# Optimization experiments

Hardware: AMD Instinct MI355X
Metric: run time of the kernel (lower is better)

Reference implementation:

```python
import math
import jax, jax.numpy as jnp
import numpy as np

B, C, H, W = 4, 64, 128, 128
A = 64           # attention_size
OUT = 64         # output_size
KS = 3           # kernel_size
M = (KS - 1) // 2
SCALE = A ** (-0.5)


def _lin(x, Wt, b):
    return x @ Wt + b


def _pos_encoding(d_model, seq_len):
    # sinusoidal PE over the k^2 neighborhood positions; d_model even here
    pos = jnp.arange(seq_len, dtype=jnp.float32)[:, None]
    div = jnp.exp(jnp.arange(0, d_model, 2, dtype=jnp.float32) * (-math.log(10000.0) / d_model))
    s = jnp.sin(pos * div)   # (seq, d/2)
    c = jnp.cos(pos * div)
    return jnp.stack([s, c], axis=-1).reshape(seq_len, d_model)  # interleaved sin/cos


def _expand_shift(k_nchw):
    # k_nchw: (b, c, h, w) -> (b, c, h, w, KS*KS) neighbor gather (zero padded)
    h, w = k_nchw.shape[2], k_nchw.shape[3]
    p = jnp.pad(k_nchw, ((0, 0), (0, 0), (M, M), (M, M)))
    slices = [p[:, :, i:i + h, j:j + w] for i in range(KS) for j in range(KS)]
    return jnp.stack(slices, axis=-1)


def setup_inputs() -> dict:
    key = jax.random.key(0)
    ks = jax.random.split(key, 12)
    sd = lambda fan_in: 1.0 / math.sqrt(fan_in)
    return {
        "x": jax.random.normal(ks[0], (B, C, H, W), jnp.float32),
        "ln_g": jnp.ones((C,), jnp.float32),
        "ln_b": jnp.zeros((C,), jnp.float32),
        "Wq": jax.random.normal(ks[1], (C, 2 * A), jnp.float32) * sd(C),
        "bq": jnp.zeros((2 * A,), jnp.float32),
        "Wq2": jax.random.normal(ks[2], (2 * A, A), jnp.float32) * sd(2 * A),
        "bq2": jnp.zeros((A,), jnp.float32),
        "Wk": jax.random.normal(ks[3], (C, 2 * A), jnp.float32) * sd(C),
        "bk": jnp.zeros((2 * A,), jnp.float32),
        "Wk2": jax.random.normal(ks[4], (2 * A, A), jnp.float32) * sd(2 * A),
        "bk2": jnp.zeros((A,), jnp.float32),
        "Wv": jax.random.normal(ks[5], (C, 2 * A), jnp.float32) * sd(C),
        "bv": jnp.zeros((2 * A,), jnp.float32),
        "Wv2": jax.random.normal(ks[6], (2 * A, OUT), jnp.float32) * sd(2 * A),
        "bv2": jnp.zeros((OUT,), jnp.float32),
        "Wpos": jax.random.normal(ks[7], (C, A), jnp.float32) * sd(C),
        "bpos": jnp.zeros((A,), jnp.float32),
        "Wposk": jax.random.normal(ks[8], (A, A), jnp.float32) * sd(A),
        "bposk": jnp.zeros((A,), jnp.float32),
    }


def reference(x, ln_g, ln_b, Wq, bq, Wq2, bq2, Wk, bk, Wk2, bk2,
              Wv, bv, Wv2, bv2, Wpos, bpos, Wposk, bposk):
    # positional embedding over the 9 neighborhood slots
    pe = _pos_encoding(C, KS * KS)                       # (9, C)
    pos_emb = jax.nn.relu(_lin(pe, Wpos, bpos))          # (9, A)

    xn = jnp.transpose(x, (0, 2, 3, 1))                  # (b, h, w, c)
    mu = jnp.mean(xn, axis=-1, keepdims=True)
    var = jnp.mean((xn - mu) ** 2, axis=-1, keepdims=True)
    xn = (xn - mu) * jax.lax.rsqrt(var + 1e-5) * ln_g + ln_b

    K = _lin(jax.nn.relu(_lin(xn, Wk, bk)), Wk2, bk2)    # (b, h, w, A)
    Ksh = _expand_shift(jnp.transpose(K, (0, 3, 1, 2)))  # (b, A, h, w, 9)
    pos_k = jnp.transpose(_lin(pos_emb, Wposk, bposk))   # (A, 9)
    Kfull = Ksh + pos_k[None, :, None, None, :]

    Q = _lin(jax.nn.relu(_lin(xn, Wq, bq)), Wq2, bq2)    # (b, h, w, A)
    V = _lin(jax.nn.relu(_lin(xn, Wv, bv)), Wv2, bv2)    # (b, h, w, OUT)
    Vsh = _expand_shift(jnp.transpose(V, (0, 3, 1, 2)))  # (b, OUT, h, w, 9)

    att = jnp.einsum('bhwa,bahwp->bphw', Q, Kfull) * SCALE
    att = jax.nn.softmax(att, axis=1)                    # softmax over 9 neighbors
    out = jnp.einsum('bchwn,bnhw->bchw', Vsh, att)       # (b, OUT, h, w)
    return out  # stride == 1 -> no subsampling
```

## Files before the change

kernel.cpp:

```cpp
#include <hip/hip_runtime.h>
#include <hip/hip_bf16.h>
#include <math.h>

typedef __attribute__((ext_vector_type(8))) short short8;
typedef __attribute__((ext_vector_type(4))) float float4v;
typedef unsigned short ushort_t;
typedef unsigned int uint_t;

#define HWPIX 16384
#define NPIX  65536

__device__ inline float b2f(ushort_t u) {
    uint_t x = ((uint_t)u) << 16;
    return __builtin_bit_cast(float, x);
}
__device__ inline ushort_t f2b(float f) {
    uint_t x = __builtin_bit_cast(uint_t, f);
    uint_t r = (x + 0x7fffu + ((x >> 16) & 1u)) >> 16;
    return (ushort_t)r;
}
__device__ inline uint_t pack2(float a, float b) {
    return (uint_t)f2b(a) | ((uint_t)f2b(b) << 16);
}
__device__ inline bool probe_bf16(const void* lng) {
    return *(const uint_t*)lng == 0x3F803F80u;
}
__device__ inline float ldf(const void* p, int i, bool bf) {
    return bf ? b2f(((const ushort_t*)p)[i]) : ((const float*)p)[i];
}
__device__ inline void unpack8(uint4 u, float* f) {
    f[0] = b2f((ushort_t)(u.x & 0xffff)); f[1] = b2f((ushort_t)(u.x >> 16));
    f[2] = b2f((ushort_t)(u.y & 0xffff)); f[3] = b2f((ushort_t)(u.y >> 16));
    f[4] = b2f((ushort_t)(u.z & 0xffff)); f[5] = b2f((ushort_t)(u.z >> 16));
    f[6] = b2f((ushort_t)(u.w & 0xffff)); f[7] = b2f((ushort_t)(u.w >> 16));
}

__global__ __launch_bounds__(256) void prep_kernel(
        const void* __restrict__ Wq, const void* __restrict__ Wq2,
        const void* __restrict__ Wk, const void* __restrict__ Wk2,
        const void* __restrict__ Wv, const void* __restrict__ Wv2,
        const void* __restrict__ Wpos, const void* __restrict__ bpos,
        const void* __restrict__ Wposk, const void* __restrict__ bposk,
        const void* __restrict__ lng,
        ushort_t* __restrict__ W1A, ushort_t* __restrict__ W2A, float* __restrict__ pk) {
    bool bf = probe_bf16(lng);
    if (blockIdx.x < 96) {
        int idx = blockIdx.x * 256 + threadIdx.x;
        int chain = idx >> 13;
        int o = idx & 8191;
        const void* W1 = chain == 0 ? Wq : (chain == 1 ? Wk : Wv);
        const void* W2 = chain == 0 ? Wq2 : (chain == 1 ? Wk2 : Wv2);
        {
            int j = o & 7, L = (o >> 3) & 63, kc = (o >> 9) & 1, mt = (o >> 10) & 7;
            int k = kc * 32 + ((L >> 4) << 3) + j;
            int m = mt * 16 + (L & 15);
            W1A[chain * 8192 + o] = f2b(ldf(W1, k * 128 + m, bf));
        }
        {
            int j = o & 7, L = (o >> 3) & 63, kc = (o >> 9) & 3, mt2 = (o >> 11) & 3;
            int k = kc * 32 + ((L >> 4) << 3) + j;
            int m = mt2 * 16 + (L & 15);
            W2A[chain * 8192 + o] = f2b(ldf(W2, k * 64 + m, bf));
        }
    } else {
        __shared__ float pe[9][64];
        __shared__ float pemb[9][64];
        int t = threadIdx.x;
        for (int it = t; it < 576; it += 256) {
            int p = it >> 6, a = it & 63;
            int i = a >> 1;
            float div = expf(-(float)(2 * i) * 0.14391156831212787f);
            float ang = (float)p * div;
            pe[p][a] = (a & 1) ? cosf(ang) : sinf(ang);
        }
        __syncthreads();
        for (int it = t; it < 576; it += 256) {
            int p = it >> 6, a = it & 63;
            float s = ldf(bpos, a, bf);
            for (int c = 0; c < 64; ++c) s += pe[p][c] * ldf(Wpos, c * 64 + a, bf);
            pemb[p][a] = fmaxf(s, 0.f);
        }
        __syncthreads();
        for (int it = t; it < 576; it += 256) {
            int p = it >> 6, a = it & 63;
            float s = ldf(bposk, a, bf);
            for (int j = 0; j < 64; ++j) s += pemb[p][j] * ldf(Wposk, j * 64 + a, bf);
            pk[a * 9 + p] = s;
        }
    }
}

__global__ __launch_bounds__(256) void lnqkv_kernel(
        const void* __restrict__ x, const void* __restrict__ g, const void* __restrict__ bb,
        const ushort_t* __restrict__ W1A, const ushort_t* __restrict__ W2A,
        const void* __restrict__ b1q, const void* __restrict__ b1k, const void* __restrict__ b1v,
        const void* __restrict__ b2q, const void* __restrict__ b2k, const void* __restrict__ b2v,
        const void* __restrict__ lng,
        ushort_t* __restrict__ Qo, ushort_t* __restrict__ Ko, ushort_t* __restrict__ Vo) {
    bool bf = probe_bf16(lng);
    int tid = threadIdx.x;
    int wave = tid >> 6, lane = tid & 63;
    int q = lane >> 4, r = lane & 15;
    int base = blockIdx.x * 256 + wave * 64;
    int b = base >> 14;
    int spBase = base & 16383;

    short8 bfr[4][2];
#pragma unroll
    for (int t = 0; t < 4; ++t) {
        int sp = spBase + t * 16 + r;
        float xl[8], xh[8];
        if (bf) {
            const ushort_t* xb = (const ushort_t*)x + (size_t)b * 64 * HWPIX + sp;
#pragma unroll
            for (int j = 0; j < 8; ++j) {
                xl[j] = b2f(xb[(size_t)(q * 8 + j) * HWPIX]);
                xh[j] = b2f(xb[(size_t)(32 + q * 8 + j) * HWPIX]);
            }
        } else {
            const float* xb = (const float*)x + (size_t)b * 64 * HWPIX + sp;
#pragma unroll
            for (int j = 0; j < 8; ++j) {
                xl[j] = xb[(size_t)(q * 8 + j) * HWPIX];
                xh[j] = xb[(size_t)(32 + q * 8 + j) * HWPIX];
            }
        }
        float s1 = 0.f, s2 = 0.f;
#pragma unroll
        for (int j = 0; j < 8; ++j) {
            s1 += xl[j] + xh[j];
            s2 += xl[j] * xl[j] + xh[j] * xh[j];
        }
        s1 += __shfl_xor(s1, 16); s2 += __shfl_xor(s2, 16);
        s1 += __shfl_xor(s1, 32); s2 += __shfl_xor(s2, 32);
        float mu = s1 * (1.f / 64.f);
        float var = s2 * (1.f / 64.f) - mu * mu;
        float rstd = rsqrtf(var + 1e-5f);
#pragma unroll
        for (int j = 0; j < 8; ++j) {
            int c = q * 8 + j;
            bfr[t][0][j] = (short)f2b((xl[j] - mu) * rstd * ldf(g, c, bf) + ldf(bb, c, bf));
            bfr[t][1][j] = (short)f2b((xh[j] - mu) * rstd * ldf(g, c + 32, bf) + ldf(bb, c + 32, bf));
        }
    }

    __shared__ __align__(16) ushort_t hid[4][4][16][128];

#pragma unroll 1
    for (int chain = 0; chain < 3; ++chain) {
        const ushort_t* W1 = W1A + chain * 8192;
        const ushort_t* W2 = W2A + chain * 8192;
        const void* b1 = chain == 0 ? b1q : (chain == 1 ? b1k : b1v);
        const void* b2 = chain == 0 ? b2q : (chain == 1 ? b2k : b2v);
        ushort_t* out = chain == 0 ? Qo : (chain == 1 ? Ko : Vo);

        {
            short8 w1[8][2];
#pragma unroll
            for (int mt = 0; mt < 8; ++mt)
#pragma unroll
                for (int kc = 0; kc < 2; ++kc)
                    w1[mt][kc] = *reinterpret_cast<const short8*>(W1 + ((mt * 2 + kc) * 64 + lane) * 8);
#pragma unroll
            for (int mt = 0; mt < 8; ++mt) {
                float bias0 = ldf(b1, mt * 16 + q * 4 + 0, bf);
                float bias1 = ldf(b1, mt * 16 + q * 4 + 1, bf);
                float bias2 = ldf(b1, mt * 16 + q * 4 + 2, bf);
                float bias3 = ldf(b1, mt * 16 + q * 4 + 3, bf);
#pragma unroll
                for (int t = 0; t < 4; ++t) {
                    float4v acc = {0.f, 0.f, 0.f, 0.f};
                    acc = __builtin_amdgcn_mfma_f32_16x16x32_bf16(w1[mt][0], bfr[t][0], acc, 0, 0, 0);
                    acc = __builtin_amdgcn_mfma_f32_16x16x32_bf16(w1[mt][1], bfr[t][1], acc, 0, 0, 0);
                    float v0 = fmaxf(acc[0] + bias0, 0.f);
                    float v1 = fmaxf(acc[1] + bias1, 0.f);
                    float v2 = fmaxf(acc[2] + bias2, 0.f);
                    float v3 = fmaxf(acc[3] + bias3, 0.f);
                    int chunk = (2 * mt + (q >> 1)) ^ r;
                    ushort_t* dst = &hid[wave][t][r][0] + chunk * 8 + (q & 1) * 4;
                    uint2 d; d.x = pack2(v0, v1); d.y = pack2(v2, v3);
                    *reinterpret_cast<uint2*>(dst) = d;
                }
            }
        }
        {
            short8 w2[4][4];
#pragma unroll
            for (int mt2 = 0; mt2 < 4; ++mt2)
#pragma unroll
                for (int kc = 0; kc < 4; ++kc)
                    w2[mt2][kc] = *reinterpret_cast<const short8*>(W2 + ((mt2 * 4 + kc) * 64 + lane) * 8);
            short8 h2[4][4];
#pragma unroll
            for (int t = 0; t < 4; ++t)
#pragma unroll
                for (int kc = 0; kc < 4; ++kc) {
                    int chunk = (4 * kc + q) ^ r;
                    h2[t][kc] = *reinterpret_cast<const short8*>(&hid[wave][t][r][0] + chunk * 8);
                }
#pragma unroll
            for (int mt2 = 0; mt2 < 4; ++mt2) {
                float bias0 = ldf(b2, mt2 * 16 + q * 4 + 0, bf);
                float bias1 = ldf(b2, mt2 * 16 + q * 4 + 1, bf);
                float bias2 = ldf(b2, mt2 * 16 + q * 4 + 2, bf);
                float bias3 = ldf(b2, mt2 * 16 + q * 4 + 3, bf);
#pragma unroll
                for (int t = 0; t < 4; ++t) {
                    float4v acc = {0.f, 0.f, 0.f, 0.f};
#pragma unroll
                    for (int kc = 0; kc < 4; ++kc)
                        acc = __builtin_amdgcn_mfma_f32_16x16x32_bf16(w2[mt2][kc], h2[t][kc], acc, 0, 0, 0);
                    uint2 d;
                    d.x = pack2(acc[0] + bias0, acc[1] + bias1);
                    d.y = pack2(acc[2] + bias2, acc[3] + bias3);
                    int pixel = base + t * 16 + r;
                    *reinterpret_cast<uint2*>(out + (size_t)pixel * 64 + mt2 * 16 + q * 4) = d;
                }
            }
        }
    }
}

__global__ __launch_bounds__(256) void attn_kernel(
        const ushort_t* __restrict__ Q, const ushort_t* __restrict__ K,
        const ushort_t* __restrict__ V, const float* __restrict__ pk,
        const void* __restrict__ lng, void* __restrict__ out) {
    bool bf = probe_bf16(lng);
    int p = blockIdx.x * 256 + threadIdx.x;
    int b = p >> 14;
    int sp = p & 16383;
    int h = sp >> 7, w = sp & 127;

    float v64[64];
    const ushort_t* qp = Q + (size_t)p * 64;
#pragma unroll
    for (int c0 = 0; c0 < 64; c0 += 8) {
        uint4 u = *reinterpret_cast<const uint4*>(qp + c0);
        unpack8(u, &v64[c0]);
    }

    float s[9];
#pragma unroll
    for (int n = 0; n < 9; ++n) {
        int dy = n / 3 - 1, dx = n % 3 - 1;
        int hh = h + dy, ww = w + dx;
        float dot = 0.f;
#pragma unroll
        for (int c = 0; c < 64; ++c) dot += v64[c] * pk[c * 9 + n];
        if (hh >= 0 && hh < 128 && ww >= 0 && ww < 128) {
            const ushort_t* kp = K + ((size_t)(b << 14) + (size_t)(hh * 128 + ww)) * 64;
#pragma unroll
            for (int c0 = 0; c0 < 64; c0 += 8) {
                uint4 u = *reinterpret_cast<const uint4*>(kp + c0);
                float kv[8];
                unpack8(u, kv);
#pragma unroll
                for (int j = 0; j < 8; ++j) dot += v64[c0 + j] * kv[j];
            }
        }
        s[n] = dot * 0.125f;
    }
    float m = s[0];
#pragma unroll
    for (int n = 1; n < 9; ++n) m = fmaxf(m, s[n]);
    float sum = 0.f;
#pragma unroll
    for (int n = 0; n < 9; ++n) { s[n] = expf(s[n] - m); sum += s[n]; }
    float inv = 1.f / sum;

#pragma unroll
    for (int c = 0; c < 64; ++c) v64[c] = 0.f;
#pragma unroll
    for (int n = 0; n < 9; ++n) {
        int dy = n / 3 - 1, dx = n % 3 - 1;
        int hh = h + dy, ww = w + dx;
        if (hh < 0 || hh >= 128 || ww < 0 || ww >= 128) continue;
        float a = s[n] * inv;
        const ushort_t* vp = V + ((size_t)(b << 14) + (size_t)(hh * 128 + ww)) * 64;
#pragma unroll
        for (int c0 = 0; c0 < 64; c0 += 8) {
            uint4 u = *reinterpret_cast<const uint4*>(vp + c0);
            float vv[8];
            unpack8(u, vv);
#pragma unroll
            for (int j = 0; j < 8; ++j) v64[c0 + j] += a * vv[j];
        }
    }
    if (bf) {
        ushort_t* ob = (ushort_t*)out + ((size_t)b * 64) * HWPIX + sp;
#pragma unroll
        for (int c = 0; c < 64; ++c) ob[(size_t)c * HWPIX] = f2b(v64[c]);
    } else {
        float* ob = (float*)out + ((size_t)b * 64) * HWPIX + sp;
#pragma unroll
        for (int c = 0; c < 64; ++c) ob[(size_t)c * HWPIX] = v64[c];
    }
}

extern "C" void kernel_launch(void* const* d_in, const int* in_sizes, int n_in,
                              void* d_out, int out_size, void* d_ws, size_t ws_size,
                              hipStream_t stream) {
    (void)in_sizes; (void)n_in; (void)out_size; (void)ws_size;
    const void* x     = d_in[0];
    const void* ln_g  = d_in[1];
    const void* ln_b  = d_in[2];
    const void* Wq    = d_in[3];
    const void* bq    = d_in[4];
    const void* Wq2   = d_in[5];
    const void* bq2   = d_in[6];
    const void* Wk    = d_in[7];
    const void* bk    = d_in[8];
    const void* Wk2   = d_in[9];
    const void* bk2   = d_in[10];
    const void* Wv    = d_in[11];
    const void* bv    = d_in[12];
    const void* Wv2   = d_in[13];
    const void* bv2   = d_in[14];
    const void* Wpos  = d_in[15];
    const void* bpos  = d_in[16];
    const void* Wposk = d_in[17];
    const void* bposk = d_in[18];

    char* ws = (char*)d_ws;
    ushort_t* Qo  = (ushort_t*)(ws);
    ushort_t* Ko  = (ushort_t*)(ws + (size_t)8 * 1024 * 1024);
    ushort_t* Vo  = (ushort_t*)(ws + (size_t)16 * 1024 * 1024);
    ushort_t* W1A = (ushort_t*)(ws + (size_t)24 * 1024 * 1024);
    ushort_t* W2A = (ushort_t*)(ws + (size_t)24 * 1024 * 1024 + 65536);
    float*    pk  = (float*)(ws + (size_t)24 * 1024 * 1024 + 131072);

    prep_kernel<<<97, 256, 0, stream>>>(Wq, Wq2, Wk, Wk2, Wv, Wv2,
                                        Wpos, bpos, Wposk, bposk, ln_g, W1A, W2A, pk);
    lnqkv_kernel<<<256, 256, 0, stream>>>(x, ln_g, ln_b, W1A, W2A,
                                          bq, bk, bv, bq2, bk2, bv2, ln_g, Qo, Ko, Vo);
    attn_kernel<<<256, 256, 0, stream>>>(Qo, Ko, Vo, pk, ln_g, d_out);
}
```

Baseline: 177.9 us.

## Compute positional Q·posK scores via MFMA in QKV kernel, halve pixels per block

Moves the per-pixel dot product of Q with the 9 positional key vectors out of the attention kernel's scalar loop and into the QKV kernel. There it is computed with two bf16 MFMAs from the Q tile staged in shared memory and stored as a 16-float score per pixel. The QKV kernel also processes 32 pixels per wave instead of 64, doubling its grid to 512 blocks for more parallelism. The bf16 unpack helper is simplified to use bit shifts and masks. The trade-offs are an extra 4 MB buffer written and then read back, and the positional term now being rounded to bf16.

Result: no change. 176.0 us (-1.1%).

```diff
diff --git a/kernel.cpp b/kernel.cpp
--- a/kernel.cpp
+++ b/kernel.cpp
@@ -28,11 +28,13 @@
 __device__ inline float ldf(const void* p, int i, bool bf) {
     return bf ? b2f(((const ushort_t*)p)[i]) : ((const float*)p)[i];
 }
+__device__ inline float lo2f(uint_t u) { return __builtin_bit_cast(float, u << 16); }
+__device__ inline float hi2f(uint_t u) { return __builtin_bit_cast(float, u & 0xffff0000u); }
 __device__ inline void unpack8(uint4 u, float* f) {
-    f[0] = b2f((ushort_t)(u.x & 0xffff)); f[1] = b2f((ushort_t)(u.x >> 16));
-    f[2] = b2f((ushort_t)(u.y & 0xffff)); f[3] = b2f((ushort_t)(u.y >> 16));
-    f[4] = b2f((ushort_t)(u.z & 0xffff)); f[5] = b2f((ushort_t)(u.z >> 16));
-    f[6] = b2f((ushort_t)(u.w & 0xffff)); f[7] = b2f((ushort_t)(u.w >> 16));
+    f[0] = lo2f(u.x); f[1] = hi2f(u.x);
+    f[2] = lo2f(u.y); f[3] = hi2f(u.y);
+    f[4] = lo2f(u.z); f[5] = hi2f(u.z);
+    f[6] = lo2f(u.w); f[7] = hi2f(u.w);
 }
 
 __global__ __launch_bounds__(256) void prep_kernel(
@@ -42,7 +44,7 @@
         const void* __restrict__ Wpos, const void* __restrict__ bpos,
         const void* __restrict__ Wposk, const void* __restrict__ bposk,
         const void* __restrict__ lng,
-        ushort_t* __restrict__ W1A, ushort_t* __restrict__ W2A, float* __restrict__ pk) {
+        ushort_t* __restrict__ W1A, ushort_t* __restrict__ W2A, ushort_t* __restrict__ pkA) {
     bool bf = probe_bf16(lng);
     if (blockIdx.x < 96) {
         int idx = blockIdx.x * 256 + threadIdx.x;
@@ -65,6 +67,7 @@
     } else {
         __shared__ float pe[9][64];
         __shared__ float pemb[9][64];
+        __shared__ float pks[64][9];
         int t = threadIdx.x;
         for (int it = t; it < 576; it += 256) {
             int p = it >> 6, a = it & 63;
@@ -85,7 +88,17 @@
             int p = it >> 6, a = it & 63;
             float s = ldf(bposk, a, bf);
             for (int j = 0; j < 64; ++j) s += pemb[p][j] * ldf(Wposk, j * 64 + a, bf);
-            pk[a * 9 + p] = s;
+            pks[a][p] = s;
+        }
+        __syncthreads();
+        if (t < 128) {
+            int kc = t >> 6, L = t & 63;
+            int m = L & 15;
+#pragma unroll
+            for (int j = 0; j < 8; ++j) {
+                int k = kc * 32 + ((L >> 4) << 3) + j;
+                pkA[(kc * 64 + L) * 8 + j] = (m < 9) ? f2b(pks[k][m]) : (ushort_t)0;
+            }
         }
     }
 }
@@ -93,21 +106,26 @@
 __global__ __launch_bounds__(256) void lnqkv_kernel(
         const void* __restrict__ x, const void* __restrict__ g, const void* __restrict__ bb,
         const ushort_t* __restrict__ W1A, const ushort_t* __restrict__ W2A,
+        const ushort_t* __restrict__ pkAp,
         const void* __restrict__ b1q, const void* __restrict__ b1k, const void* __restrict__ b1v,
         const void* __restrict__ b2q, const void* __restrict__ b2k, const void* __restrict__ b2v,
         const void* __restrict__ lng,
-        ushort_t* __restrict__ Qo, ushort_t* __restrict__ Ko, ushort_t* __restrict__ Vo) {
+        ushort_t* __restrict__ Qo, ushort_t* __restrict__ Ko, ushort_t* __restrict__ Vo,
+        float* __restrict__ Spos) {
     bool bf = probe_bf16(lng);
     int tid = threadIdx.x;
     int wave = tid >> 6, lane = tid & 63;
     int q = lane >> 4, r = lane & 15;
-    int base = blockIdx.x * 256 + wave * 64;
+    int base = blockIdx.x * 128 + wave * 32;
     int b = base >> 14;
     int spBase = base & 16383;
 
-    short8 bfr[4][2];
-#pragma unroll
-    for (int t = 0; t < 4; ++t) {
+    short8 pkA0 = *reinterpret_cast<const short8*>(pkAp + (0 * 64 + lane) * 8);
+    short8 pkA1 = *reinterpret_cast<const short8*>(pkAp + (1 * 64 + lane) * 8);
+
+    short8 bfr[2][2];
+#pragma unroll
+    for (int t = 0; t < 2; ++t) {
         int sp = spBase + t * 16 + r;
         float xl[8], xh[8];
         if (bf) {
@@ -144,7 +162,7 @@
         }
     }
 
-    __shared__ __align__(16) ushort_t hid[4][4][16][128];
+    __shared__ __align__(16) ushort_t hid[4][2][16][128];
 
 #pragma unroll 1
     for (int chain = 0; chain < 3; ++chain) {
@@ -168,7 +186,7 @@
                 float bias2 = ldf(b1, mt * 16 + q * 4 + 2, bf);
                 float bias3 = ldf(b1, mt * 16 + q * 4 + 3, bf);
 #pragma unroll
-                for (int t = 0; t < 4; ++t) {
+                for (int t = 0; t < 2; ++t) {
                     float4v acc = {0.f, 0.f, 0.f, 0.f};
                     acc = __builtin_amdgcn_mfma_f32_16x16x32_bf16(w1[mt][0], bfr[t][0], acc, 0, 0, 0);
                     acc = __builtin_amdgcn_mfma_f32_16x16x32_bf16(w1[mt][1], bfr[t][1], acc, 0, 0, 0);
@@ -190,9 +208,9 @@
 #pragma unroll
                 for (int kc = 0; kc < 4; ++kc)
                     w2[mt2][kc] = *reinterpret_cast<const short8*>(W2 + ((mt2 * 4 + kc) * 64 + lane) * 8);
-            short8 h2[4][4];
-#pragma unroll
-            for (int t = 0; t < 4; ++t)
+            short8 h2[2][4];
+#pragma unroll
+            for (int t = 0; t < 2; ++t)
 #pragma unroll
                 for (int kc = 0; kc < 4; ++kc) {
                     int chunk = (4 * kc + q) ^ r;
@@ -205,7 +223,7 @@
                 float bias2 = ldf(b2, mt2 * 16 + q * 4 + 2, bf);
                 float bias3 = ldf(b2, mt2 * 16 + q * 4 + 3, bf);
 #pragma unroll
-                for (int t = 0; t < 4; ++t) {
+                for (int t = 0; t < 2; ++t) {
                     float4v acc = {0.f, 0.f, 0.f, 0.f};
 #pragma unroll
                     for (int kc = 0; kc < 4; ++kc)
@@ -215,7 +233,33 @@
                     d.y = pack2(acc[2] + bias2, acc[3] + bias3);
                     int pixel = base + t * 16 + r;
                     *reinterpret_cast<uint2*>(out + (size_t)pixel * 64 + mt2 * 16 + q * 4) = d;
-                }
+                    if (chain == 0) {
+                        int chunk = (2 * mt2 + (q >> 1)) ^ r;
+                        ushort_t* dst = &hid[wave][t][r][0] + chunk * 8 + (q & 1) * 4;
+                        *reinterpret_cast<uint2*>(dst) = d;
+                    }
+                }
+            }
+        }
+        if (chain == 0) {
+#pragma unroll
+            for (int t = 0; t < 2; ++t) {
+                short8 qB0, qB1;
+                {
+                    int chunk = (4 * 0 + q) ^ r;
+                    qB0 = *reinterpret_cast<const short8*>(&hid[wave][t][r][0] + chunk * 8);
+                }
+                {
+                    int chunk = (4 * 1 + q) ^ r;
+                    qB1 = *reinterpret_cast<const short8*>(&hid[wave][t][r][0] + chunk * 8);
+                }
+                float4v acc = {0.f, 0.f, 0.f, 0.f};
+                acc = __builtin_amdgcn_mfma_f32_16x16x32_bf16(pkA0, qB0, acc, 0, 0, 0);
+                acc = __builtin_amdgcn_mfma_f32_16x16x32_bf16(pkA1, qB1, acc, 0, 0, 0);
+                int pixel = base + t * 16 + r;
+                float4 o;
+                o.x = acc[0]; o.y = acc[1]; o.z = acc[2]; o.w = acc[3];
+                *reinterpret_cast<float4*>(Spos + (size_t)pixel * 16 + q * 4) = o;
             }
         }
     }
@@ -223,7 +267,7 @@
 
 __global__ __launch_bounds__(256) void attn_kernel(
         const ushort_t* __restrict__ Q, const ushort_t* __restrict__ K,
-        const ushort_t* __restrict__ V, const float* __restrict__ pk,
+        const ushort_t* __restrict__ V, const float* __restrict__ Spos,
         const void* __restrict__ lng, void* __restrict__ out) {
     bool bf = probe_bf16(lng);
     int p = blockIdx.x * 256 + threadIdx.x;
@@ -240,13 +284,18 @@
     }
 
     float s[9];
+    {
+        float4 s0 = *reinterpret_cast<const float4*>(Spos + (size_t)p * 16);
+        float4 s1 = *reinterpret_cast<const float4*>(Spos + (size_t)p * 16 + 4);
+        s[0] = s0.x; s[1] = s0.y; s[2] = s0.z; s[3] = s0.w;
+        s[4] = s1.x; s[5] = s1.y; s[6] = s1.z; s[7] = s1.w;
+        s[8] = Spos[(size_t)p * 16 + 8];
+    }
 #pragma unroll
     for (int n = 0; n < 9; ++n) {
         int dy = n / 3 - 1, dx = n % 3 - 1;
         int hh = h + dy, ww = w + dx;
         float dot = 0.f;
-#pragma unroll
-        for (int c = 0; c < 64; ++c) dot += v64[c] * pk[c * 9 + n];
         if (hh >= 0 && hh < 128 && ww >= 0 && ww < 128) {
             const ushort_t* kp = K + ((size_t)(b << 14) + (size_t)(hh * 128 + ww)) * 64;
 #pragma unroll
@@ -258,7 +307,7 @@
                 for (int j = 0; j < 8; ++j) dot += v64[c0 + j] * kv[j];
             }
         }
-        s[n] = dot * 0.125f;
+        s[n] = (s[n] + dot) * 0.125f;
     }
     float m = s[0];
 #pragma unroll
@@ -322,16 +371,17 @@
     const void* bposk = d_in[18];
 
     char* ws = (char*)d_ws;
-    ushort_t* Qo  = (ushort_t*)(ws);
-    ushort_t* Ko  = (ushort_t*)(ws + (size_t)8 * 1024 * 1024);
-    ushort_t* Vo  = (ushort_t*)(ws + (size_t)16 * 1024 * 1024);
-    ushort_t* W1A = (ushort_t*)(ws + (size_t)24 * 1024 * 1024);
-    ushort_t* W2A = (ushort_t*)(ws + (size_t)24 * 1024 * 1024 + 65536);
-    float*    pk  = (float*)(ws + (size_t)24 * 1024 * 1024 + 131072);
+    ushort_t* Qo   = (ushort_t*)(ws);
+    ushort_t* Ko   = (ushort_t*)(ws + (size_t)8 * 1024 * 1024);
+    ushort_t* Vo   = (ushort_t*)(ws + (size_t)16 * 1024 * 1024);
+    float*    Spos = (float*)(ws + (size_t)24 * 1024 * 1024);
+    ushort_t* W1A  = (ushort_t*)(ws + (size_t)28 * 1024 * 1024);
+    ushort_t* W2A  = (ushort_t*)(ws + (size_t)28 * 1024 * 1024 + 65536);
+    ushort_t* pkA  = (ushort_t*)(ws + (size_t)28 * 1024 * 1024 + 131072);
 
     prep_kernel<<<97, 256, 0, stream>>>(Wq, Wq2, Wk, Wk2, Wv, Wv2,
-                                        Wpos, bpos, Wposk, bposk, ln_g, W1A, W2A, pk);
-    lnqkv_kernel<<<256, 256, 0, stream>>>(x, ln_g, ln_b, W1A, W2A,
-                                          bq, bk, bv, bq2, bk2, bv2, ln_g, Qo, Ko, Vo);
-    attn_kernel<<<256, 256, 0, stream>>>(Qo, Ko, Vo, pk, ln_g, d_out);
-}
+                                        Wpos, bpos, Wposk, bposk, ln_g, W1A, W2A, pkA);
+    lnqkv_kernel<<<512, 256, 0, stream>>>(x, ln_g, ln_b, W1A, W2A, pkA,
+                                          bq, bk, bv, bq2, bk2, bv2, ln_g, Qo, Ko, Vo, Spos);
+    attn_kernel<<<256, 256, 0, stream>>>(Qo, Ko, Vo, Spos, ln_g, d_out);
+}
```

## Fuse LN/QKV projection and neighborhood attention into one tiled kernel with halo

Applied to the files above, without the earlier changes.

Merges the QKV projection kernel and the attention kernel into one kernel. Each block handles a 16x16 spatial tile plus a one-pixel halo and keeps Q, K and V in swizzled LDS, so the global Q/K/V intermediates and their round trip through memory go away. The positional-key term is now computed with an MFMA against a prepacked pk matrix instead of a scalar 64-wide dot per neighbor. The cost is recomputing projections for halo pixels (about 27% extra MFMA work), only one block per CU because of the large LDS footprint, and just 256 blocks.

New measurement: 182.1 us. +2.4%, slower.

```diff
diff --git a/kernel.cpp b/kernel.cpp
--- a/kernel.cpp
+++ b/kernel.cpp
@@ -8,7 +8,9 @@
 typedef unsigned int uint_t;
 
 #define HWPIX 16384
-#define NPIX  65536
+#define SLOTS 324
+#define NTILES 21
+#define ROWS 336
 
 __device__ inline float b2f(ushort_t u) {
     uint_t x = ((uint_t)u) << 16;
@@ -28,11 +30,13 @@
 __device__ inline float ldf(const void* p, int i, bool bf) {
     return bf ? b2f(((const ushort_t*)p)[i]) : ((const float*)p)[i];
 }
+__device__ inline float lo2f(uint_t u) { return __builtin_bit_cast(float, u << 16); }
+__device__ inline float hi2f(uint_t u) { return __builtin_bit_cast(float, u & 0xffff0000u); }
 __device__ inline void unpack8(uint4 u, float* f) {
-    f[0] = b2f((ushort_t)(u.x & 0xffff)); f[1] = b2f((ushort_t)(u.x >> 16));
-    f[2] = b2f((ushort_t)(u.y & 0xffff)); f[3] = b2f((ushort_t)(u.y >> 16));
-    f[4] = b2f((ushort_t)(u.z & 0xffff)); f[5] = b2f((ushort_t)(u.z >> 16));
-    f[6] = b2f((ushort_t)(u.w & 0xffff)); f[7] = b2f((ushort_t)(u.w >> 16));
+    f[0] = lo2f(u.x); f[1] = hi2f(u.x);
+    f[2] = lo2f(u.y); f[3] = hi2f(u.y);
+    f[4] = lo2f(u.z); f[5] = hi2f(u.z);
+    f[6] = lo2f(u.w); f[7] = hi2f(u.w);
 }
 
 __global__ __launch_bounds__(256) void prep_kernel(
@@ -42,7 +46,7 @@
         const void* __restrict__ Wpos, const void* __restrict__ bpos,
         const void* __restrict__ Wposk, const void* __restrict__ bposk,
         const void* __restrict__ lng,
-        ushort_t* __restrict__ W1A, ushort_t* __restrict__ W2A, float* __restrict__ pk) {
+        ushort_t* __restrict__ W1A, ushort_t* __restrict__ W2A, ushort_t* __restrict__ pkA) {
     bool bf = probe_bf16(lng);
     if (blockIdx.x < 96) {
         int idx = blockIdx.x * 256 + threadIdx.x;
@@ -65,6 +69,7 @@
     } else {
         __shared__ float pe[9][64];
         __shared__ float pemb[9][64];
+        __shared__ float pks[64][9];
         int t = threadIdx.x;
         for (int it = t; it < 576; it += 256) {
             int p = it >> 6, a = it & 63;
@@ -85,45 +90,71 @@
             int p = it >> 6, a = it & 63;
             float s = ldf(bposk, a, bf);
             for (int j = 0; j < 64; ++j) s += pemb[p][j] * ldf(Wposk, j * 64 + a, bf);
-            pk[a * 9 + p] = s;
-        }
-    }
-}
-
-__global__ __launch_bounds__(256) void lnqkv_kernel(
+            pks[a][p] = s;
+        }
+        __syncthreads();
+        if (t < 128) {
+            int kc = t >> 6, L = t & 63;
+            int m = L & 15;
+#pragma unroll
+            for (int j = 0; j < 8; ++j) {
+                int k = kc * 32 + ((L >> 4) << 3) + j;
+                pkA[(kc * 64 + L) * 8 + j] = (m < 9) ? f2b(pks[k][m]) : (ushort_t)0;
+            }
+        }
+    }
+}
+
+__global__ __launch_bounds__(256, 1) void fused_kernel(
         const void* __restrict__ x, const void* __restrict__ g, const void* __restrict__ bb,
         const ushort_t* __restrict__ W1A, const ushort_t* __restrict__ W2A,
+        const ushort_t* __restrict__ pkAp,
         const void* __restrict__ b1q, const void* __restrict__ b1k, const void* __restrict__ b1v,
         const void* __restrict__ b2q, const void* __restrict__ b2k, const void* __restrict__ b2v,
-        const void* __restrict__ lng,
-        ushort_t* __restrict__ Qo, ushort_t* __restrict__ Ko, ushort_t* __restrict__ Vo) {
+        const void* __restrict__ lng, void* __restrict__ out) {
+    __shared__ __align__(16) ushort_t xq[ROWS][64];
+    __shared__ __align__(16) ushort_t KL[ROWS][64];
+    __shared__ __align__(16) ushort_t VL[ROWS][64];
+    __shared__ __align__(16) ushort_t hid[4][16][128];
+    __shared__ float SposL[SLOTS][9];
+
     bool bf = probe_bf16(lng);
     int tid = threadIdx.x;
     int wave = tid >> 6, lane = tid & 63;
     int q = lane >> 4, r = lane & 15;
-    int base = blockIdx.x * 256 + wave * 64;
-    int b = base >> 14;
-    int spBase = base & 16383;
-
-    short8 bfr[4][2];
-#pragma unroll
-    for (int t = 0; t < 4; ++t) {
-        int sp = spBase + t * 16 + r;
+    int blk = blockIdx.x;
+    int b = blk >> 6, ty = (blk >> 3) & 7, tx = blk & 7;
+    int gy0 = ty * 16 - 1, gx0 = tx * 16 - 1;
+    const size_t xoff = (size_t)b * 64 * HWPIX;
+
+    short8 pkA0 = *reinterpret_cast<const short8*>(pkAp + (0 * 64 + lane) * 8);
+    short8 pkA1 = *reinterpret_cast<const short8*>(pkAp + (1 * 64 + lane) * 8);
+
+    for (int t = wave; t < NTILES; t += 4) {
+        int s = t * 16 + r;
+        int hy = s / 18, hx = s - hy * 18;
+        int gy = gy0 + hy, gx = gx0 + hx;
+        bool valid = (s < SLOTS) && (gy >= 0) && (gy < 128) && (gx >= 0) && (gx < 128);
         float xl[8], xh[8];
-        if (bf) {
-            const ushort_t* xb = (const ushort_t*)x + (size_t)b * 64 * HWPIX + sp;
-#pragma unroll
-            for (int j = 0; j < 8; ++j) {
-                xl[j] = b2f(xb[(size_t)(q * 8 + j) * HWPIX]);
-                xh[j] = b2f(xb[(size_t)(32 + q * 8 + j) * HWPIX]);
+        if (valid) {
+            if (bf) {
+                const ushort_t* xb = (const ushort_t*)x + xoff + (size_t)(gy * 128 + gx);
+#pragma unroll
+                for (int j = 0; j < 8; ++j) {
+                    xl[j] = b2f(xb[(size_t)(q * 8 + j) * HWPIX]);
+                    xh[j] = b2f(xb[(size_t)(32 + q * 8 + j) * HWPIX]);
+                }
+            } else {
+                const float* xb = (const float*)x + xoff + (size_t)(gy * 128 + gx);
+#pragma unroll
+                for (int j = 0; j < 8; ++j) {
+                    xl[j] = xb[(size_t)(q * 8 + j) * HWPIX];
+                    xh[j] = xb[(size_t)(32 + q * 8 + j) * HWPIX];
+                }
             }
         } else {
-            const float* xb = (const float*)x + (size_t)b * 64 * HWPIX + sp;
-#pragma unroll
-            for (int j = 0; j < 8; ++j) {
-                xl[j] = xb[(size_t)(q * 8 + j) * HWPIX];
-                xh[j] = xb[(size_t)(32 + q * 8 + j) * HWPIX];
-            }
+#pragma unroll
+            for (int j = 0; j < 8; ++j) { xl[j] = 0.f; xh[j] = 0.f; }
         }
         float s1 = 0.f, s2 = 0.f;
 #pragma unroll
@@ -136,162 +167,157 @@
         float mu = s1 * (1.f / 64.f);
         float var = s2 * (1.f / 64.f) - mu * mu;
         float rstd = rsqrtf(var + 1e-5f);
+        short8 a0, a1;
 #pragma unroll
         for (int j = 0; j < 8; ++j) {
             int c = q * 8 + j;
-            bfr[t][0][j] = (short)f2b((xl[j] - mu) * rstd * ldf(g, c, bf) + ldf(bb, c, bf));
-            bfr[t][1][j] = (short)f2b((xh[j] - mu) * rstd * ldf(g, c + 32, bf) + ldf(bb, c + 32, bf));
-        }
-    }
-
-    __shared__ __align__(16) ushort_t hid[4][4][16][128];
+            a0[j] = (short)f2b((xl[j] - mu) * rstd * ldf(g, c, bf) + ldf(bb, c, bf));
+            a1[j] = (short)f2b((xh[j] - mu) * rstd * ldf(g, c + 32, bf) + ldf(bb, c + 32, bf));
+        }
+        int sw = r & 7;
+        *reinterpret_cast<short8*>(&xq[s][(q ^ sw) * 8]) = a0;
+        *reinterpret_cast<short8*>(&xq[s][((4 + q) ^ sw) * 8]) = a1;
+    }
 
 #pragma unroll 1
-    for (int chain = 0; chain < 3; ++chain) {
+    for (int c3 = 0; c3 < 3; ++c3) {
+        int chain = (c3 == 0) ? 1 : (c3 == 1) ? 2 : 0;
         const ushort_t* W1 = W1A + chain * 8192;
         const ushort_t* W2 = W2A + chain * 8192;
         const void* b1 = chain == 0 ? b1q : (chain == 1 ? b1k : b1v);
         const void* b2 = chain == 0 ? b2q : (chain == 1 ? b2k : b2v);
-        ushort_t* out = chain == 0 ? Qo : (chain == 1 ? Ko : Vo);
-
-        {
-            short8 w1[8][2];
-#pragma unroll
-            for (int mt = 0; mt < 8; ++mt)
-#pragma unroll
-                for (int kc = 0; kc < 2; ++kc)
-                    w1[mt][kc] = *reinterpret_cast<const short8*>(W1 + ((mt * 2 + kc) * 64 + lane) * 8);
+
+        short8 w1[8][2];
+#pragma unroll
+        for (int mt = 0; mt < 8; ++mt)
+#pragma unroll
+            for (int kc = 0; kc < 2; ++kc)
+                w1[mt][kc] = *reinterpret_cast<const short8*>(W1 + ((mt * 2 + kc) * 64 + lane) * 8);
+        short8 w2[4][4];
+#pragma unroll
+        for (int mt2 = 0; mt2 < 4; ++mt2)
+#pragma unroll
+            for (int kc = 0; kc < 4; ++kc)
+                w2[mt2][kc] = *reinterpret_cast<const short8*>(W2 + ((mt2 * 4 + kc) * 64 + lane) * 8);
+
+        for (int t = wave; t < NTILES; t += 4) {
+            int s = t * 16 + r;
+            int sw = r & 7;
+            int hy = s / 18, hx = s - hy * 18;
+            int gy = gy0 + hy, gx = gx0 + hx;
+            bool valid = (s < SLOTS) && (gy >= 0) && (gy < 128) && (gx >= 0) && (gx < 128);
+
+            short8 xb0 = *reinterpret_cast<const short8*>(&xq[s][(q ^ sw) * 8]);
+            short8 xb1 = *reinterpret_cast<const short8*>(&xq[s][((4 + q) ^ sw) * 8]);
+
 #pragma unroll
             for (int mt = 0; mt < 8; ++mt) {
-                float bias0 = ldf(b1, mt * 16 + q * 4 + 0, bf);
-                float bias1 = ldf(b1, mt * 16 + q * 4 + 1, bf);
-                float bias2 = ldf(b1, mt * 16 + q * 4 + 2, bf);
-                float bias3 = ldf(b1, mt * 16 + q * 4 + 3, bf);
-#pragma unroll
-                for (int t = 0; t < 4; ++t) {
-                    float4v acc = {0.f, 0.f, 0.f, 0.f};
-                    acc = __builtin_amdgcn_mfma_f32_16x16x32_bf16(w1[mt][0], bfr[t][0], acc, 0, 0, 0);
-                    acc = __builtin_amdgcn_mfma_f32_16x16x32_bf16(w1[mt][1], bfr[t][1], acc, 0, 0, 0);
-                    float v0 = fmaxf(acc[0] + bias0, 0.f);
-                    float v1 = fmaxf(acc[1] + bias1, 0.f);
-                    float v2 = fmaxf(acc[2] + bias2, 0.f);
-                    float v3 = fmaxf(acc[3] + bias3, 0.f);
-                    int chunk = (2 * mt + (q >> 1)) ^ r;
-                    ushort_t* dst = &hid[wave][t][r][0] + chunk * 8 + (q & 1) * 4;
-                    uint2 d; d.x = pack2(v0, v1); d.y = pack2(v2, v3);
-                    *reinterpret_cast<uint2*>(dst) = d;
+                float4v acc = {0.f, 0.f, 0.f, 0.f};
+                acc = __builtin_amdgcn_mfma_f32_16x16x32_bf16(w1[mt][0], xb0, acc, 0, 0, 0);
+                acc = __builtin_amdgcn_mfma_f32_16x16x32_bf16(w1[mt][1], xb1, acc, 0, 0, 0);
+                float v0 = fmaxf(acc[0] + ldf(b1, mt * 16 + q * 4 + 0, bf), 0.f);
+                float v1 = fmaxf(acc[1] + ldf(b1, mt * 16 + q * 4 + 1, bf), 0.f);
+                float v2 = fmaxf(acc[2] + ldf(b1, mt * 16 + q * 4 + 2, bf), 0.f);
+                float v3 = fmaxf(acc[3] + ldf(b1, mt * 16 + q * 4 + 3, bf), 0.f);
+                uint2 d; d.x = pack2(v0, v1); d.y = pack2(v2, v3);
+                int chunk = (2 * mt + (q >> 1)) ^ r;
+                *reinterpret_cast<uint2*>(&hid[wave][r][chunk * 8 + (q & 1) * 4]) = d;
+            }
+            short8 h2[4];
+#pragma unroll
+            for (int kc = 0; kc < 4; ++kc)
+                h2[kc] = *reinterpret_cast<const short8*>(&hid[wave][r][((4 * kc + q) ^ r) * 8]);
+            ushort_t* rowp = (c3 == 0) ? &KL[s][0] : (c3 == 1) ? &VL[s][0] : &xq[s][0];
+#pragma unroll
+            for (int mt2 = 0; mt2 < 4; ++mt2) {
+                float4v acc = {0.f, 0.f, 0.f, 0.f};
+#pragma unroll
+                for (int kc = 0; kc < 4; ++kc)
+                    acc = __builtin_amdgcn_mfma_f32_16x16x32_bf16(w2[mt2][kc], h2[kc], acc, 0, 0, 0);
+                uint2 d;
+                d.x = pack2(acc[0] + ldf(b2, mt2 * 16 + q * 4 + 0, bf),
+                            acc[1] + ldf(b2, mt2 * 16 + q * 4 + 1, bf));
+                d.y = pack2(acc[2] + ldf(b2, mt2 * 16 + q * 4 + 2, bf),
+                            acc[3] + ldf(b2, mt2 * 16 + q * 4 + 3, bf));
+                if (c3 < 2 && !valid) { d.x = 0u; d.y = 0u; }
+                int chunk = (2 * mt2 + (q >> 1)) ^ sw;
+                *reinterpret_cast<uint2*>(&rowp[chunk * 8 + (q & 1) * 4]) = d;
+            }
+            if (c3 == 2) {
+                short8 qB0 = *reinterpret_cast<const short8*>(&xq[s][(q ^ sw) * 8]);
+                short8 qB1 = *reinterpret_cast<const short8*>(&xq[s][((4 + q) ^ sw) * 8]);
+                float4v acc = {0.f, 0.f, 0.f, 0.f};
+                acc = __builtin_amdgcn_mfma_f32_16x16x32_bf16(pkA0, qB0, acc, 0, 0, 0);
+                acc = __builtin_amdgcn_mfma_f32_16x16x32_bf16(pkA1, qB1, acc, 0, 0, 0);
+                if (s < SLOTS) {
+#pragma unroll
+                    for (int rr = 0; rr < 4; ++rr) {
+                        int n = q * 4 + rr;
+                        if (n < 9) SposL[s][n] = acc[rr];
+                    }
                 }
             }
         }
-        {
-            short8 w2[4][4];
-#pragma unroll
-            for (int mt2 = 0; mt2 < 4; ++mt2)
-#pragma unroll
-                for (int kc = 0; kc < 4; ++kc)
-                    w2[mt2][kc] = *reinterpret_cast<const short8*>(W2 + ((mt2 * 4 + kc) * 64 + lane) * 8);
-            short8 h2[4][4];
-#pragma unroll
-            for (int t = 0; t < 4; ++t)
-#pragma unroll
-                for (int kc = 0; kc < 4; ++kc) {
-                    int chunk = (4 * kc + q) ^ r;
-                    h2[t][kc] = *reinterpret_cast<const short8*>(&hid[wave][t][r][0] + chunk * 8);
-                }
-#pragma unroll
-            for (int mt2 = 0; mt2 < 4; ++mt2) {
-                float bias0 = ldf(b2, mt2 * 16 + q * 4 + 0, bf);
-                float bias1 = ldf(b2, mt2 * 16 + q * 4 + 1, bf);
-                float bias2 = ldf(b2, mt2 * 16 + q * 4 + 2, bf);
-                float bias3 = ldf(b2, mt2 * 16 + q * 4 + 3, bf);
-#pragma unroll
-                for (int t = 0; t < 4; ++t) {
-                    float4v acc = {0.f, 0.f, 0.f, 0.f};
-#pragma unroll
-                    for (int kc = 0; kc < 4; ++kc)
-                        acc = __builtin_amdgcn_mfma_f32_16x16x32_bf16(w2[mt2][kc], h2[t][kc], acc, 0, 0, 0);
-                    uint2 d;
-                    d.x = pack2(acc[0] + bias0, acc[1] + bias1);
-                    d.y = pack2(acc[2] + bias2, acc[3] + bias3);
-                    int pixel = base + t * 16 + r;
-                    *reinterpret_cast<uint2*>(out + (size_t)pixel * 64 + mt2 * 16 + q * 4) = d;
-                }
-            }
-        }
-    }
-}
-
-__global__ __launch_bounds__(256) void attn_kernel(
-        const ushort_t* __restrict__ Q, const ushort_t* __restrict__ K,
-        const ushort_t* __restrict__ V, const float* __restrict__ pk,
-        const void* __restrict__ lng, void* __restrict__ out) {
-    bool bf = probe_bf16(lng);
-    int p = blockIdx.x * 256 + threadIdx.x;
-    int b = p >> 14;
-    int sp = p & 16383;
-    int h = sp >> 7, w = sp & 127;
-
+    }
+    __syncthreads();
+
+    int iy = tid >> 4, ix = tid & 15;
+    int s0 = (iy + 1) * 18 + (ix + 1);
+    int sw0 = s0 & 7;
     float v64[64];
-    const ushort_t* qp = Q + (size_t)p * 64;
-#pragma unroll
-    for (int c0 = 0; c0 < 64; c0 += 8) {
-        uint4 u = *reinterpret_cast<const uint4*>(qp + c0);
-        unpack8(u, &v64[c0]);
-    }
-
-    float s[9];
+#pragma unroll
+    for (int g8 = 0; g8 < 8; ++g8) {
+        uint4 u = *reinterpret_cast<const uint4*>(&xq[s0][(g8 ^ sw0) * 8]);
+        unpack8(u, &v64[g8 * 8]);
+    }
+    float sc[9];
+#pragma unroll
+    for (int n = 0; n < 9; ++n) sc[n] = SposL[s0][n];
 #pragma unroll
     for (int n = 0; n < 9; ++n) {
-        int dy = n / 3 - 1, dx = n % 3 - 1;
-        int hh = h + dy, ww = w + dx;
+        int sk = s0 + (n / 3 - 1) * 18 + (n % 3 - 1);
+        int swk = sk & 7;
         float dot = 0.f;
 #pragma unroll
-        for (int c = 0; c < 64; ++c) dot += v64[c] * pk[c * 9 + n];
-        if (hh >= 0 && hh < 128 && ww >= 0 && ww < 128) {
-            const ushort_t* kp = K + ((size_t)(b << 14) + (size_t)(hh * 128 + ww)) * 64;
-#pragma unroll
-            for (int c0 = 0; c0 < 64; c0 += 8) {
-                uint4 u = *reinterpret_cast<const uint4*>(kp + c0);
-                float kv[8];
-                unpack8(u, kv);
-#pragma unroll
-                for (int j = 0; j < 8; ++j) dot += v64[c0 + j] * kv[j];
-            }
-        }
-        s[n] = dot * 0.125f;
-    }
-    float m = s[0];
-#pragma unroll
-    for (int n = 1; n < 9; ++n) m = fmaxf(m, s[n]);
+        for (int g8 = 0; g8 < 8; ++g8) {
+            uint4 u = *reinterpret_cast<const uint4*>(&KL[sk][(g8 ^ swk) * 8]);
+            float kv[8];
+            unpack8(u, kv);
+#pragma unroll
+            for (int j = 0; j < 8; ++j) dot += v64[g8 * 8 + j] * kv[j];
+        }
+        sc[n] = (sc[n] + dot) * 0.125f;
+    }
+    float m = sc[0];
+#pragma unroll
+    for (int n = 1; n < 9; ++n) m = fmaxf(m, sc[n]);
     float sum = 0.f;
 #pragma unroll
-    for (int n = 0; n < 9; ++n) { s[n] = expf(s[n] - m); sum += s[n]; }
+    for (int n = 0; n < 9; ++n) { sc[n] = expf(sc[n] - m); sum += sc[n]; }
     float inv = 1.f / sum;
-
 #pragma unroll
     for (int c = 0; c < 64; ++c) v64[c] = 0.f;
 #pragma unroll
     for (int n = 0; n < 9; ++n) {
-        int dy = n / 3 - 1, dx = n % 3 - 1;
-        int hh = h + dy, ww = w + dx;
-        if (hh < 0 || hh >= 128 || ww < 0 || ww >= 128) continue;
-        float a = s[n] * inv;
-        const ushort_t* vp = V + ((size_t)(b << 14) + (size_t)(hh * 128 + ww)) * 64;
-#pragma unroll
-        for (int c0 = 0; c0 < 64; c0 += 8) {
-            uint4 u = *reinterpret_cast<const uint4*>(vp + c0);
+        int sk = s0 + (n / 3 - 1) * 18 + (n % 3 - 1);
+        int swk = sk & 7;
+        float a = sc[n] * inv;
+#pragma unroll
+        for (int g8 = 0; g8 < 8; ++g8) {
+            uint4 u = *reinterpret_cast<const uint4*>(&VL[sk][(g8 ^ swk) * 8]);
             float vv[8];
             unpack8(u, vv);
 #pragma unroll
-            for (int j = 0; j < 8; ++j) v64[c0 + j] += a * vv[j];
-        }
-    }
+            for (int j = 0; j < 8; ++j) v64[g8 * 8 + j] += a * vv[j];
+        }
+    }
+    int gy = ty * 16 + iy, gx = tx * 16 + ix;
     if (bf) {
-        ushort_t* ob = (ushort_t*)out + ((size_t)b * 64) * HWPIX + sp;
+        ushort_t* ob = (ushort_t*)out + xoff + (size_t)(gy * 128 + gx);
 #pragma unroll
         for (int c = 0; c < 64; ++c) ob[(size_t)c * HWPIX] = f2b(v64[c]);
     } else {
-        float* ob = (float*)out + ((size_t)b * 64) * HWPIX + sp;
+        float* ob = (float*)out + xoff + (size_t)(gy * 128 + gx);
 #pragma unroll
         for (int c = 0; c < 64; ++c) ob[(size_t)c * HWPIX] = v64[c];
     }
@@ -322,16 +348,12 @@
     const void* bposk = d_in[18];
 
     char* ws = (char*)d_ws;
-    ushort_t* Qo  = (ushort_t*)(ws);
-    ushort_t* Ko  = (ushort_t*)(ws + (size_t)8 * 1024 * 1024);
-    ushort_t* Vo  = (ushort_t*)(ws + (size_t)16 * 1024 * 1024);
-    ushort_t* W1A = (ushort_t*)(ws + (size_t)24 * 1024 * 1024);
-    ushort_t* W2A = (ushort_t*)(ws + (size_t)24 * 1024 * 1024 + 65536);
-    float*    pk  = (float*)(ws + (size_t)24 * 1024 * 1024 + 131072);
+    ushort_t* W1A = (ushort_t*)(ws);
+    ushort_t* W2A = (ushort_t*)(ws + 65536);
+    ushort_t* pkA = (ushort_t*)(ws + 131072);
 
     prep_kernel<<<97, 256, 0, stream>>>(Wq, Wq2, Wk, Wk2, Wv, Wv2,
-                                        Wpos, bpos, Wposk, bposk, ln_g, W1A, W2A, pk);
-    lnqkv_kernel<<<256, 256, 0, stream>>>(x, ln_g, ln_b, W1A, W2A,
-                                          bq, bk, bv, bq2, bk2, bv2, ln_g, Qo, Ko, Vo);
-    attn_kernel<<<256, 256, 0, stream>>>(Qo, Ko, Vo, pk, ln_g, d_out);
-}
+                                        Wpos, bpos, Wposk, bposk, ln_g, W1A, W2A, pkA);
+    fused_kernel<<<256, 256, 0, stream>>>(x, ln_g, ln_b, W1A, W2A, pkA,
+                                          bq, bk, bv, bq2, bk2, bv2, ln_g, d_out);
+}
```
